# Optimization experiments

Hardware: AMD Instinct MI355X
Metric: run time of the kernel (lower is better)

## Reference

```python
import jax, jax.numpy as jnp
import numpy as np

N = 4096        # number of nodes
C = 512         # in_features
L_LAT = 64      # L_latent
EPS = 0.25      # epsilon


def setup_inputs() -> dict:
    key = jax.random.key(0)
    ks = jax.random.split(key, 8)
    def lin(k, fan_in, shape):
        return (jax.random.normal(k, shape, jnp.float32) / np.float32(np.sqrt(fan_in)))
    x = jax.random.normal(ks[0], (N, C), jnp.float32)
    adj = jax.random.uniform(ks[1], (N, N), jnp.float32)  # dense nonneg kernel
    W_proj = lin(ks[2], C, (C, L_LAT)); b_proj = jnp.zeros((L_LAT,), jnp.float32)
    W_pi1 = lin(ks[3], L_LAT, (L_LAT, C)); b_pi1 = jnp.zeros((C,), jnp.float32)
    W_pi2 = lin(ks[4], C, (C, 1)); b_pi2 = jnp.zeros((1,), jnp.float32)
    W_f = lin(ks[5], C, (C, C)); b_f = jnp.zeros((C,), jnp.float32)
    dt = jnp.array([0.1], jnp.float32)
    return {"x": x, "adj": adj, "W_proj": W_proj, "b_proj": b_proj,
            "W_pi1": W_pi1, "b_pi1": b_pi1, "W_pi2": W_pi2, "b_pi2": b_pi2,
            "W_f": W_f, "b_f": b_f, "dt": dt}


def reference(x, adj, W_proj, b_proj, W_pi1, b_pi1, W_pi2, b_pi2, W_f, b_f, dt):
    # proj_list: x -> latent [n, L]
    z = x @ W_proj + b_proj
    # pi_list: Linear -> ReLU -> Linear -> Sigmoid, squeeze to [n]
    pi = jax.nn.sigmoid(jax.nn.relu(z @ W_pi1 + b_pi1) @ W_pi2 + b_pi2)[:, 0]
    # q_epsilon_tilde: row sums of the kernel
    q = adj.sum(axis=1)                       # [n]
    # K_tilde = K_epsilon @ diag(pi/q)  == column scaling
    K_tilde = adj * (pi / q)[None, :]         # [n, n]
    # D_tilde diagonal; torch.inverse of a diagonal == elementwise reciprocal
    d = K_tilde.sum(axis=1) + 1e-5            # [n]
    # target = relu(f(x)) with f = Linear(C, C)
    target = jax.nn.relu(x @ W_f + b_f)       # [n, C]
    # L @ target = (1/eps) * diag(1/d) @ K_tilde @ target - target
    Lt = (K_tilde @ target) / (EPS * d)[:, None] - target
    return target + dt[0] * Lt
```

## Files before the change

kernel.cpp:

```cpp
#include <hip/hip_runtime.h>
#include <hip/hip_bf16.h>

#define N_NODES 4096
#define C_DIM   512
#define L_DIM   64
#define SPLITS  8
#define KCHUNK  (N_NODES / SPLITS)

typedef unsigned short u16;
typedef unsigned int   u32;
using bf16x8 = __attribute__((ext_vector_type(8))) __bf16;
using u16x8  = __attribute__((ext_vector_type(8))) unsigned short;
using f32x4  = __attribute__((ext_vector_type(4))) float;

__device__ __forceinline__ float b2f(u16 u) {
    union { unsigned int i; float f; } v; v.i = ((unsigned int)u) << 16; return v.f;
}
__device__ __forceinline__ u16 f2b(float f) {
    __bf16 h = (__bf16)f;
    union { __bf16 h; u16 u; } v; v.h = h; return v.u;
}
__device__ __forceinline__ void gload16(const void* g, void* l) {
    __builtin_amdgcn_global_load_lds((const __attribute__((address_space(1))) void*)g,
                                     (__attribute__((address_space(3))) void*)l,
                                     16, 0, 0);
}
__device__ __forceinline__ int detect_mode_inl(const u16* __restrict__ adj) {
    int m = 0;
#pragma unroll
    for (int i = 0; i < 64; ++i) m |= (adj[i] >= 0x8000) ? 1 : 0;
    return m;
}
__device__ __forceinline__ float ldin(const void* p, int i, int mode) {
    if (mode) return ((const float*)p)[i];
    return b2f(((const u16*)p)[i]);
}

#define OFF_MODE  0
#define OFF_DT    64
#define OFF_BIAS  1024
#define OFF_BP    4096
#define OFF_BP1   4608
#define OFF_WP2   8192
#define OFF_BP2   10240
#define OFF_Q     16384
#define OFF_S     32768
#define OFF_DV    49152
#define OFF_WPP   65536
#define OFF_WP1P  131072
#define OFF_WFT   196608
#define OFF_TST   9437184
#define OFF_XB    13631488
#define OFF_ADJB  17825792

__global__ __launch_bounds__(256) void k1_prep(const void* __restrict__ adj, const void* __restrict__ x,
        const void* Wp, const void* bp, const void* Wp1, const void* bp1,
        const void* Wp2, const void* bp2, const void* Wf, const void* bfc, const void* dt,
        int* __restrict__ modep,
        float* __restrict__ bp_f, float* __restrict__ bp1_f,
        float* __restrict__ Wp2_f, float* __restrict__ bp2_f,
        float* __restrict__ bias_f, float* __restrict__ dt_f,
        u32* __restrict__ WpP, u32* __restrict__ Wp1P,
        u16* __restrict__ adjb, float* __restrict__ q, u16* __restrict__ xb,
        u16* __restrict__ WfT) {
    __shared__ float tile[32][33];
    int bid = blockIdx.x, tid = threadIdx.x;
    int mode = detect_mode_inl((const u16*)adj);
    if (bid < 1024) {
        int wave = tid >> 6, lane = tid & 63;
        int row = bid * 4 + wave;
        float acc = 0.f;
        if (mode) {
            const float4* rp = (const float4*)((const float*)adj + (size_t)row * N_NODES);
            ushort4* wp = (ushort4*)(adjb + (size_t)row * N_NODES);
#pragma unroll 8
            for (int it = 0; it < 16; ++it) {
                float4 v = rp[it * 64 + lane];
                acc += (v.x + v.y) + (v.z + v.w);
                ushort4 o; o.x = f2b(v.x); o.y = f2b(v.y); o.z = f2b(v.z); o.w = f2b(v.w);
                wp[it * 64 + lane] = o;
            }
        } else {
            const u16x8* rp = (const u16x8*)((const u16*)adj + (size_t)row * N_NODES);
#pragma unroll
            for (int it = 0; it < 8; ++it) {
                u16x8 v = rp[it * 64 + lane];
#pragma unroll
                for (int e = 0; e < 8; ++e) acc += b2f(v[e]);
            }
        }
#pragma unroll
        for (int off = 32; off > 0; off >>= 1) acc += __shfl_down(acc, off);
        if (lane == 0) q[row] = acc;
    } else if (bid < 3072) {
        if (mode == 0) return;
        int idx = (bid - 1024) * 256 + tid;
        float4 v = ((const float4*)x)[idx];
        ushort4 o; o.x = f2b(v.x); o.y = f2b(v.y); o.z = f2b(v.z); o.w = f2b(v.w);
        ((ushort4*)xb)[idx] = o;
    } else if (bid < 3328) {
        int g = bid - 3072;
        int tx = tid & 31, ty = tid >> 5;
        int x0 = (g & 15) * 32, y0 = (g >> 4) * 32;
        if (mode) {
            const float* src = (const float*)Wf;
#pragma unroll
            for (int r = ty; r < 32; r += 8) tile[r][tx] = src[(size_t)(y0 + r) * C_DIM + x0 + tx];
        } else {
            const u16* src = (const u16*)Wf;
#pragma unroll
            for (int r = ty; r < 32; r += 8) tile[r][tx] = b2f(src[(size_t)(y0 + r) * C_DIM + x0 + tx]);
        }
        __syncthreads();
#pragma unroll
        for (int r = ty; r < 32; r += 8)
            WfT[(size_t)(x0 + r) * C_DIM + y0 + tx] = f2b(tile[tx][r]);
    } else if (bid < 3392) {
        int idx = (bid - 3328) * 256 + tid;
        int k2i = idx >> 6, j = idx & 63;
        float a = ldin(Wp, (2 * k2i) * L_DIM + j, mode);
        float b = ldin(Wp, (2 * k2i + 1) * L_DIM + j, mode);
        WpP[idx] = (u32)f2b(a) | ((u32)f2b(b) << 16);
    } else if (bid < 3456) {
        int idx = (bid - 3392) * 256 + tid;
        int jj2 = idx >> 9, m = idx & 511;
        float a = ldin(Wp1, (2 * jj2) * C_DIM + m, mode);
        float b = ldin(Wp1, (2 * jj2 + 1) * C_DIM + m, mode);
        Wp1P[idx] = (u32)f2b(a) | ((u32)f2b(b) << 16);
    } else {
        if (bid == 3456 && tid == 0) *modep = mode;
        int idx = (bid - 3456) * 256 + tid;
        if (idx < 64)           bp_f[idx]          = ldin(bp,  idx, mode);
        else if (idx < 576)     bp1_f[idx - 64]    = ldin(bp1, idx - 64, mode);
        else if (idx < 1088)    Wp2_f[idx - 576]   = ldin(Wp2, idx - 576, mode);
        else if (idx == 1088)   bp2_f[0]           = ldin(bp2, 0, mode);
        else if (idx < 1601)    bias_f[idx - 1089] = ldin(bfc, idx - 1089, mode);
        else if (idx == 1601)   dt_f[0]            = ldin(dt, 0, mode);
    }
}

__global__ __launch_bounds__(256) void k1p_pi(const void* __restrict__ xraw,
        const int* __restrict__ modep, const u16* __restrict__ xb,
        const u32* __restrict__ WpP, const u32* __restrict__ Wp1P,
        const float* __restrict__ bp_f,  const float* __restrict__ bp1_f,
        const float* __restrict__ Wp2_f, const float* __restrict__ bp2_f,
        const float* __restrict__ q, float* __restrict__ s) {
    __shared__ __align__(16) char smem[26880];
    int bid = blockIdx.x, tid = threadIdx.x;
    int mode = *modep;
    float (*sx)[C_DIM]      = (float(*)[C_DIM])smem;
    float (*red)[8][L_DIM]  = (float(*)[8][L_DIM])(smem + 16384);
    float (*sz)[L_DIM]      = (float(*)[L_DIM])(smem + 24576);
    float (*rw)[8]          = (float(*)[8])(smem + 26624);
    int i0 = bid * 8;
    const u16* xsrc = mode ? xb : (const u16*)xraw;
    const u16x8* xp = (const u16x8*)(xsrc + (size_t)i0 * C_DIM);
#pragma unroll
    for (int r = 0; r < 2; ++r) {
        u16x8 v = xp[tid + 256 * r];
        float* dstf = &sx[0][0] + (size_t)(tid + 256 * r) * 8;
#pragma unroll
        for (int e = 0; e < 8; ++e) dstf[e] = b2f(v[e]);
    }
    __syncthreads();
    int j = tid & 63, part = tid >> 6;
    float za[8];
#pragma unroll
    for (int n = 0; n < 8; ++n) za[n] = 0.f;
    const u32* wp = WpP + part * 4096 + j;
#pragma unroll 8
    for (int kk = 0; kk < 64; ++kk) {
        u32 w = wp[kk * 64];
        float wa = b2f((u16)(w & 0xFFFF)), wb = b2f((u16)(w >> 16));
        int k = part * 128 + kk * 2;
#pragma unroll
        for (int n = 0; n < 8; ++n) za[n] += sx[n][k] * wa + sx[n][k + 1] * wb;
    }
#pragma unroll
    for (int n = 0; n < 8; ++n) red[part][n][j] = za[n];
    __syncthreads();
#pragma unroll
    for (int r = 0; r < 2; ++r) {
        int idx = tid + r * 256; int n = idx >> 6, jj = idx & 63;
        sz[n][jj] = red[0][n][jj] + red[1][n][jj] + red[2][n][jj] + red[3][n][jj] + bp_f[jj];
    }
    __syncthreads();
    int m0 = tid, m1 = tid + 256;
    float h0[8], h1[8];
    float b0 = bp1_f[m0], b1 = bp1_f[m1];
#pragma unroll
    for (int n = 0; n < 8; ++n) { h0[n] = b0; h1[n] = b1; }
    const u32* w1p = Wp1P + m0;
#pragma unroll 4
    for (int jj2 = 0; jj2 < 32; ++jj2) {
        u32 w0 = w1p[jj2 * 512], w1 = w1p[jj2 * 512 + 256];
        float w0a = b2f((u16)(w0 & 0xFFFF)), w0b = b2f((u16)(w0 >> 16));
        float w1a = b2f((u16)(w1 & 0xFFFF)), w1b = b2f((u16)(w1 >> 16));
#pragma unroll
        for (int n = 0; n < 8; ++n) {
            float za_ = sz[n][2 * jj2], zb_ = sz[n][2 * jj2 + 1];
            h0[n] += za_ * w0a + zb_ * w0b;
            h1[n] += za_ * w1a + zb_ * w1b;
        }
    }
    float w2a = Wp2_f[m0], w2b = Wp2_f[m1];
    float p[8];
#pragma unroll
    for (int n = 0; n < 8; ++n)
        p[n] = fmaxf(h0[n], 0.f) * w2a + fmaxf(h1[n], 0.f) * w2b;
#pragma unroll
    for (int off = 32; off > 0; off >>= 1)
#pragma unroll
        for (int n = 0; n < 8; ++n) p[n] += __shfl_down(p[n], off);
    int lane = tid & 63, wave = tid >> 6;
    if (lane == 0) {
#pragma unroll
        for (int n = 0; n < 8; ++n) rw[wave][n] = p[n];
    }
    __syncthreads();
    if (tid < 8) {
        float tot = rw[0][tid] + rw[1][tid] + rw[2][tid] + rw[3][tid] + bp2_f[0];
        float pi = 1.f / (1.f + expf(-tot));
        s[i0 + tid] = pi / q[i0 + tid];
    }
}

__global__ __launch_bounds__(256) void k2_mid(const void* __restrict__ adjraw, const void* __restrict__ xraw,
        const int* __restrict__ modep,
        const float* __restrict__ s, const float* __restrict__ bias_f, const float* __restrict__ dt_f,
        const u16* __restrict__ adjb, const u16* __restrict__ xb, const u16* __restrict__ WfT,
        float* __restrict__ dv, u16* __restrict__ TsT,
        void* __restrict__ out, float* __restrict__ Pacc) {
    __shared__ __align__(16) char smem[16640];
    int bid = blockIdx.x, tid = threadIdx.x;
    int mode = *modep;
    if (bid < 1024) {
        float* s_lds = (float*)smem;
#pragma unroll
        for (int r = 0; r < 4; ++r) ((float4*)s_lds)[tid + 256 * r] = ((const float4*)s)[tid + 256 * r];
        __syncthreads();
        const u16* A = mode ? adjb : (const u16*)adjraw;
        int wave = tid >> 6, lane = tid & 63;
        int row = bid * 4 + wave;
        const u16x8* rp = (const u16x8*)(A + (size_t)row * N_NODES);
        float acc = 0.f;
#pragma unroll
        for (int it = 0; it < 8; ++it) {
            int chunk = it * 64 + lane;
            u16x8 v = rp[chunk];
            const float4* sp = (const float4*)(s_lds + chunk * 8);
            float4 s0 = sp[0], s1 = sp[1];
            acc += b2f(v[0]) * s0.x + b2f(v[1]) * s0.y + b2f(v[2]) * s0.z + b2f(v[3]) * s0.w;
            acc += b2f(v[4]) * s1.x + b2f(v[5]) * s1.y + b2f(v[6]) * s1.z + b2f(v[7]) * s1.w;
        }
#pragma unroll
        for (int off = 32; off > 0; off >>= 1) acc += __shfl_down(acc, off);
        if (lane == 0) dv[row] = 1.f / (acc + 1e-5f);
    } else {
        u16* lA = (u16*)smem;
        u16* lB = (u16*)(smem + 8192);
        u16* lT = (u16*)smem;
        float* s_row = (float*)(smem + 16384);
        int g = bid - 1024;
        int lane = tid & 63, wave = tid >> 6;
        int bm = (g & 63) * 64, bn = (g >> 6) * 64;
        if (tid < 64) s_row[tid] = s[bm + tid];
        const u16* Axb = mode ? xb : (const u16*)xraw;
        float* tgt = mode ? (float*)out : Pacc;
        int quad = lane >> 4, l15 = lane & 15;
        int wm = wave * 16;
        int trow = tid >> 3;
        int xslot = (tid & 7) ^ (trow & 7);
        const u16* Ap0 = Axb + (size_t)(bm + trow) * C_DIM + xslot * 8;
        const u16* Ap1 = Axb + (size_t)(bm + 32 + trow) * C_DIM + xslot * 8;
        const u16* Bp0 = WfT + (size_t)(bn + trow) * C_DIM + xslot * 8;
        const u16* Bp1 = WfT + (size_t)(bn + 32 + trow) * C_DIM + xslot * 8;
        f32x4 acc[4];
#pragma unroll
        for (int nt = 0; nt < 4; ++nt) acc[nt] = (f32x4){0.f, 0.f, 0.f, 0.f};
        for (int k0 = 0; k0 < C_DIM; k0 += 64) {
            gload16(Ap0 + k0, lA + tid * 8);
            gload16(Ap1 + k0, lA + 2048 + tid * 8);
            gload16(Bp0 + k0, lB + tid * 8);
            gload16(Bp1 + k0, lB + 2048 + tid * 8);
            asm volatile("s_waitcnt vmcnt(0)\n\ts_barrier" ::: "memory");
            __builtin_amdgcn_sched_barrier(0);
#pragma unroll
            for (int kk = 0; kk < 2; ++kk) {
                int xr = (((kk << 2) | quad) ^ (l15 & 7)) * 8;
                bf16x8 af = *(const bf16x8*)&lA[(wm + l15) * 64 + xr];
                bf16x8 bfv[4];
#pragma unroll
                for (int nt = 0; nt < 4; ++nt)
                    bfv[nt] = *(const bf16x8*)&lB[(nt * 16 + l15) * 64 + xr];
#pragma unroll
                for (int nt = 0; nt < 4; ++nt)
                    acc[nt] = __builtin_amdgcn_mfma_f32_16x16x32_bf16(af, bfv[nt], acc[nt], 0, 0, 0);
            }
            asm volatile("s_waitcnt lgkmcnt(0)\n\ts_barrier" ::: "memory");
        }
        float c0 = 1.f - dt_f[0];
#pragma unroll
        for (int nt = 0; nt < 4; ++nt) {
            int col_l = nt * 16 + l15;
            float bv = bias_f[bn + col_l];
#pragma unroll
            for (int r = 0; r < 4; ++r) {
                int row_l = wm + quad * 4 + r;
                float t = fmaxf(acc[nt][r] + bv, 0.f);
                tgt[(size_t)(bm + row_l) * C_DIM + bn + col_l] = c0 * t;
                lT[col_l * 64 + row_l] = f2b(t * s_row[row_l]);
            }
        }
        __syncthreads();
        int col_l = tid >> 2, seg = tid & 3;
        uint4 w0 = *(const uint4*)&lT[col_l * 64 + seg * 16];
        uint4 w1 = *(const uint4*)&lT[col_l * 64 + seg * 16 + 8];
        u16* dst = TsT + (size_t)(bn + col_l) * N_NODES + bm + seg * 16;
        *(uint4*)dst = w0;
        *(uint4*)(dst + 8) = w1;
    }
}

__global__ __launch_bounds__(256) void k3_gemm2(const void* __restrict__ adjraw,
        const int* __restrict__ modep,
        const u16* __restrict__ adjb, const u16* __restrict__ TsT,
        const float* __restrict__ dv, const float* __restrict__ dt_f,
        void* __restrict__ out, float* __restrict__ Pacc) {
    __shared__ __align__(16) u16 lA[8192];
    __shared__ __align__(16) u16 lB[8192];
    int mode = *modep;
    const u16* A = mode ? adjb : (const u16*)adjraw;
    float* tgt = mode ? (float*)out : Pacc;
    int tid = threadIdx.x;
    int lane = tid & 63, wave = tid >> 6;
    int id = blockIdx.x;
    int nid = (id & 7) * 128 + (id >> 3);
    int kbase = (nid & 7) * KCHUNK;
    int bn = ((nid >> 3) & 3) * 128;
    int bm = (nid >> 5) * 128;
    int wm = (wave & 1) * 64, wn = (wave >> 1) * 64;
    int quad = lane >> 4, l15 = lane & 15;
    int trow = tid >> 3;
    int xslot = (tid & 7) ^ (trow & 7);

    const u16* Ap[4]; const u16* Bp[4];
#pragma unroll
    for (int i = 0; i < 4; ++i) {
        Ap[i] = A   + (size_t)(bm + i * 32 + trow) * N_NODES + kbase + xslot * 8;
        Bp[i] = TsT + (size_t)(bn + i * 32 + trow) * N_NODES + kbase + xslot * 8;
    }

    f32x4 acc[4][4];
#pragma unroll
    for (int a = 0; a < 4; ++a)
#pragma unroll
        for (int b = 0; b < 4; ++b) acc[a][b] = (f32x4){0.f, 0.f, 0.f, 0.f};

    for (int k0 = 0; k0 < KCHUNK; k0 += 64) {
#pragma unroll
        for (int i = 0; i < 4; ++i) gload16(Ap[i] + k0, lA + i * 2048 + tid * 8);
#pragma unroll
        for (int i = 0; i < 4; ++i) gload16(Bp[i] + k0, lB + i * 2048 + tid * 8);
        asm volatile("s_waitcnt vmcnt(0)\n\ts_barrier" ::: "memory");
        __builtin_amdgcn_sched_barrier(0);
#pragma unroll
        for (int kk = 0; kk < 2; ++kk) {
            int xr = (((kk << 2) | quad) ^ (l15 & 7)) * 8;
            bf16x8 af[4], bfv[4];
#pragma unroll
            for (int mt = 0; mt < 4; ++mt) af[mt] = *(const bf16x8*)&lA[(wm + mt * 16 + l15) * 64 + xr];
#pragma unroll
            for (int nt = 0; nt < 4; ++nt) bfv[nt] = *(const bf16x8*)&lB[(wn + nt * 16 + l15) * 64 + xr];
#pragma unroll
            for (int mt = 0; mt < 4; ++mt)
#pragma unroll
                for (int nt = 0; nt < 4; ++nt)
                    acc[mt][nt] = __builtin_amdgcn_mfma_f32_16x16x32_bf16(af[mt], bfv[nt], acc[mt][nt], 0, 0, 0);
        }
        asm volatile("s_waitcnt lgkmcnt(0)\n\ts_barrier" ::: "memory");
    }

    float c1 = dt_f[0] * 4.f;
#pragma unroll
    for (int mt = 0; mt < 4; ++mt) {
        float inv[4];
#pragma unroll
        for (int r = 0; r < 4; ++r) inv[r] = c1 * dv[bm + wm + mt * 16 + quad * 4 + r];
#pragma unroll
        for (int nt = 0; nt < 4; ++nt) {
            int col = bn + wn + nt * 16 + l15;
#pragma unroll
            for (int r = 0; r < 4; ++r) {
                int row = bm + wm + mt * 16 + quad * 4 + r;
                atomicAdd(&tgt[(size_t)row * C_DIM + col], acc[mt][nt][r] * inv[r]);
            }
        }
    }
}

__global__ __launch_bounds__(256) void k5_fin(const int* __restrict__ modep,
                                              const float* __restrict__ Pacc,
                                              u16* __restrict__ out) {
    if (*modep) return;
    int idx = blockIdx.x * 256 + threadIdx.x;
    float4 v = ((const float4*)Pacc)[idx];
    ushort4 o; o.x = f2b(v.x); o.y = f2b(v.y); o.z = f2b(v.z); o.w = f2b(v.w);
    ((ushort4*)out)[idx] = o;
}

extern "C" void kernel_launch(void* const* d_in, const int* in_sizes, int n_in,
                              void* d_out, int out_size, void* d_ws, size_t ws_size,
                              hipStream_t stream) {
    const void* x   = d_in[0];
    const void* adj = d_in[1];
    const void* Wp  = d_in[2];
    const void* bp  = d_in[3];
    const void* Wp1 = d_in[4];
    const void* bp1 = d_in[5];
    const void* Wp2 = d_in[6];
    const void* bp2 = d_in[7];
    const void* Wf  = d_in[8];
    const void* bfc = d_in[9];
    const void* dtp = d_in[10];

    char* ws = (char*)d_ws;
    int*   modep  = (int*)(ws + OFF_MODE);
    float* dt_f   = (float*)(ws + OFF_DT);
    float* bias_f = (float*)(ws + OFF_BIAS);
    float* bp_f   = (float*)(ws + OFF_BP);
    float* bp1_f  = (float*)(ws + OFF_BP1);
    float* Wp2_f  = (float*)(ws + OFF_WP2);
    float* bp2_f  = (float*)(ws + OFF_BP2);
    float* q      = (float*)(ws + OFF_Q);
    float* s      = (float*)(ws + OFF_S);
    float* dv     = (float*)(ws + OFF_DV);
    u32*   WpP    = (u32*)(ws + OFF_WPP);
    u32*   Wp1P   = (u32*)(ws + OFF_WP1P);
    u16*   WfT    = (u16*)(ws + OFF_WFT);
    u16*   TsT    = (u16*)(ws + OFF_TST);
    u16*   xb     = (u16*)(ws + OFF_XB);
    u16*   adjb   = (u16*)(ws + OFF_ADJB);
    float* Pacc   = (float*)(ws + OFF_ADJB);

    k1_prep<<<3463, 256, 0, stream>>>(adj, x, Wp, bp, Wp1, bp1, Wp2, bp2, Wf, bfc, dtp,
                                      modep, bp_f, bp1_f, Wp2_f, bp2_f, bias_f, dt_f,
                                      WpP, Wp1P, adjb, q, xb, WfT);
    k1p_pi<<<512, 256, 0, stream>>>(x, modep, xb, WpP, Wp1P, bp_f, bp1_f, Wp2_f, bp2_f, q, s);
    k2_mid<<<1536, 256, 0, stream>>>(adj, x, modep, s, bias_f, dt_f, adjb, xb, WfT,
                                     dv, TsT, d_out, Pacc);
    k3_gemm2<<<1024, 256, 0, stream>>>(adj, modep, adjb, TsT, dv, dt_f, d_out, Pacc);
    k5_fin<<<2048, 256, 0, stream>>>(modep, Pacc, (u16*)d_out);
}
```

Baseline: 240.2 us.

## Fuse row-scaled reduction into GEMM2 pass and defer 1/d scaling to finalizer

Moves the K_tilde row-sum reduction (dv) from the mid kernel into extra blocks of the adjacency GEMM, accumulated with atomics, so the adj read for dv overlaps with the GEMM instead of running before it. GEMM2 now atomically accumulates unscaled partial products into a separate fp32 buffer, and the finalizer applies the per-row 1/d scale and adds the base term. Split-K is reduced from 8 to 4, giving 512 GEMM blocks plus 128 reduction blocks. The cost is zero-initialising the accumulator buffers in the prep kernel and always running a full finalizer pass, including in fp32 mode.

```diff
diff --git a/kernel.cpp b/kernel.cpp
--- a/kernel.cpp
+++ b/kernel.cpp
@@ -4,7 +4,7 @@
 #define N_NODES 4096
 #define C_DIM   512
 #define L_DIM   64
-#define SPLITS  8
+#define SPLITS  4
 #define KCHUNK  (N_NODES / SPLITS)
 
 typedef unsigned short u16;
@@ -49,6 +49,7 @@
 #define OFF_WPP   65536
 #define OFF_WP1P  131072
 #define OFF_WFT   196608
+#define OFF_PACC  720896
 #define OFF_TST   9437184
 #define OFF_XB    13631488
 #define OFF_ADJB  17825792
@@ -62,7 +63,7 @@
         float* __restrict__ bias_f, float* __restrict__ dt_f,
         u32* __restrict__ WpP, u32* __restrict__ Wp1P,
         u16* __restrict__ adjb, float* __restrict__ q, u16* __restrict__ xb,
-        u16* __restrict__ WfT) {
+        u16* __restrict__ WfT, float* __restrict__ Pacc2, float* __restrict__ dvraw) {
     __shared__ float tile[32][33];
     int bid = blockIdx.x, tid = threadIdx.x;
     int mode = detect_mode_inl((const u16*)adj);
@@ -127,7 +128,7 @@
         float a = ldin(Wp1, (2 * jj2) * C_DIM + m, mode);
         float b = ldin(Wp1, (2 * jj2 + 1) * C_DIM + m, mode);
         Wp1P[idx] = (u32)f2b(a) | ((u32)f2b(b) << 16);
-    } else {
+    } else if (bid < 3463) {
         if (bid == 3456 && tid == 0) *modep = mode;
         int idx = (bid - 3456) * 256 + tid;
         if (idx < 64)           bp_f[idx]          = ldin(bp,  idx, mode);
@@ -136,6 +137,12 @@
         else if (idx == 1088)   bp2_f[0]           = ldin(bp2, 0, mode);
         else if (idx < 1601)    bias_f[idx - 1089] = ldin(bfc, idx - 1089, mode);
         else if (idx == 1601)   dt_f[0]            = ldin(dt, 0, mode);
+    } else if (bid < 5511) {
+        int idx = (bid - 3463) * 256 + tid;
+        ((float4*)Pacc2)[idx] = make_float4(0.f, 0.f, 0.f, 0.f);
+    } else {
+        int idx = (bid - 5511) * 256 + tid;
+        dvraw[idx] = 0.f;
     }
 }
 
@@ -225,188 +232,199 @@
     }
 }
 
-__global__ __launch_bounds__(256) void k2_mid(const void* __restrict__ adjraw, const void* __restrict__ xraw,
+__global__ __launch_bounds__(256) void k2_gemm1(const void* __restrict__ xraw,
         const int* __restrict__ modep,
         const float* __restrict__ s, const float* __restrict__ bias_f, const float* __restrict__ dt_f,
-        const u16* __restrict__ adjb, const u16* __restrict__ xb, const u16* __restrict__ WfT,
-        float* __restrict__ dv, u16* __restrict__ TsT,
-        void* __restrict__ out, float* __restrict__ Pacc) {
+        const u16* __restrict__ xb, const u16* __restrict__ WfT,
+        u16* __restrict__ TsT, void* __restrict__ out, float* __restrict__ Pacc_base) {
     __shared__ __align__(16) char smem[16640];
     int bid = blockIdx.x, tid = threadIdx.x;
     int mode = *modep;
-    if (bid < 1024) {
-        float* s_lds = (float*)smem;
-#pragma unroll
-        for (int r = 0; r < 4; ++r) ((float4*)s_lds)[tid + 256 * r] = ((const float4*)s)[tid + 256 * r];
-        __syncthreads();
-        const u16* A = mode ? adjb : (const u16*)adjraw;
-        int wave = tid >> 6, lane = tid & 63;
-        int row = bid * 4 + wave;
-        const u16x8* rp = (const u16x8*)(A + (size_t)row * N_NODES);
-        float acc = 0.f;
-#pragma unroll
-        for (int it = 0; it < 8; ++it) {
-            int chunk = it * 64 + lane;
-            u16x8 v = rp[chunk];
-            const float4* sp = (const float4*)(s_lds + chunk * 8);
-            float4 s0 = sp[0], s1 = sp[1];
-            acc += b2f(v[0]) * s0.x + b2f(v[1]) * s0.y + b2f(v[2]) * s0.z + b2f(v[3]) * s0.w;
-            acc += b2f(v[4]) * s1.x + b2f(v[5]) * s1.y + b2f(v[6]) * s1.z + b2f(v[7]) * s1.w;
-        }
-#pragma unroll
-        for (int off = 32; off > 0; off >>= 1) acc += __shfl_down(acc, off);
-        if (lane == 0) dv[row] = 1.f / (acc + 1e-5f);
-    } else {
-        u16* lA = (u16*)smem;
-        u16* lB = (u16*)(smem + 8192);
-        u16* lT = (u16*)smem;
-        float* s_row = (float*)(smem + 16384);
-        int g = bid - 1024;
-        int lane = tid & 63, wave = tid >> 6;
-        int bm = (g & 63) * 64, bn = (g >> 6) * 64;
-        if (tid < 64) s_row[tid] = s[bm + tid];
-        const u16* Axb = mode ? xb : (const u16*)xraw;
-        float* tgt = mode ? (float*)out : Pacc;
-        int quad = lane >> 4, l15 = lane & 15;
-        int wm = wave * 16;
-        int trow = tid >> 3;
-        int xslot = (tid & 7) ^ (trow & 7);
-        const u16* Ap0 = Axb + (size_t)(bm + trow) * C_DIM + xslot * 8;
-        const u16* Ap1 = Axb + (size_t)(bm + 32 + trow) * C_DIM + xslot * 8;
-        const u16* Bp0 = WfT + (size_t)(bn + trow) * C_DIM + xslot * 8;
-        const u16* Bp1 = WfT + (size_t)(bn + 32 + trow) * C_DIM + xslot * 8;
-        f32x4 acc[4];
-#pragma unroll
-        for (int nt = 0; nt < 4; ++nt) acc[nt] = (f32x4){0.f, 0.f, 0.f, 0.f};
-        for (int k0 = 0; k0 < C_DIM; k0 += 64) {
-            gload16(Ap0 + k0, lA + tid * 8);
-            gload16(Ap1 + k0, lA + 2048 + tid * 8);
-            gload16(Bp0 + k0, lB + tid * 8);
-            gload16(Bp1 + k0, lB + 2048 + tid * 8);
-            asm volatile("s_waitcnt vmcnt(0)\n\ts_barrier" ::: "memory");
-            __builtin_amdgcn_sched_barrier(0);
-#pragma unroll
-            for (int kk = 0; kk < 2; ++kk) {
-                int xr = (((kk << 2) | quad) ^ (l15 & 7)) * 8;
-                bf16x8 af = *(const bf16x8*)&lA[(wm + l15) * 64 + xr];
-                bf16x8 bfv[4];
-#pragma unroll
-                for (int nt = 0; nt < 4; ++nt)
-                    bfv[nt] = *(const bf16x8*)&lB[(nt * 16 + l15) * 64 + xr];
-#pragma unroll
-                for (int nt = 0; nt < 4; ++nt)
-                    acc[nt] = __builtin_amdgcn_mfma_f32_16x16x32_bf16(af, bfv[nt], acc[nt], 0, 0, 0);
-            }
-            asm volatile("s_waitcnt lgkmcnt(0)\n\ts_barrier" ::: "memory");
-        }
-        float c0 = 1.f - dt_f[0];
-#pragma unroll
-        for (int nt = 0; nt < 4; ++nt) {
-            int col_l = nt * 16 + l15;
-            float bv = bias_f[bn + col_l];
-#pragma unroll
-            for (int r = 0; r < 4; ++r) {
-                int row_l = wm + quad * 4 + r;
-                float t = fmaxf(acc[nt][r] + bv, 0.f);
-                tgt[(size_t)(bm + row_l) * C_DIM + bn + col_l] = c0 * t;
-                lT[col_l * 64 + row_l] = f2b(t * s_row[row_l]);
-            }
-        }
-        __syncthreads();
-        int col_l = tid >> 2, seg = tid & 3;
-        uint4 w0 = *(const uint4*)&lT[col_l * 64 + seg * 16];
-        uint4 w1 = *(const uint4*)&lT[col_l * 64 + seg * 16 + 8];
-        u16* dst = TsT + (size_t)(bn + col_l) * N_NODES + bm + seg * 16;
-        *(uint4*)dst = w0;
-        *(uint4*)(dst + 8) = w1;
-    }
+    u16* lA = (u16*)smem;
+    u16* lB = (u16*)(smem + 8192);
+    u16* lT = (u16*)smem;
+    float* s_row = (float*)(smem + 16384);
+    int lane = tid & 63, wave = tid >> 6;
+    int bm = (bid & 63) * 64, bn = (bid >> 6) * 64;
+    if (tid < 64) s_row[tid] = s[bm + tid];
+    const u16* Axb = mode ? xb : (const u16*)xraw;
+    float* basep = mode ? (float*)out : Pacc_base;
+    int quad = lane >> 4, l15 = lane & 15;
+    int wm = wave * 16;
+    int trow = tid >> 3;
+    int xslot = (tid & 7) ^ (trow & 7);
+    const u16* Ap0 = Axb + (size_t)(bm + trow) * C_DIM + xslot * 8;
+    const u16* Ap1 = Axb + (size_t)(bm + 32 + trow) * C_DIM + xslot * 8;
+    const u16* Bp0 = WfT + (size_t)(bn + trow) * C_DIM + xslot * 8;
+    const u16* Bp1 = WfT + (size_t)(bn + 32 + trow) * C_DIM + xslot * 8;
+    f32x4 acc[4];
+#pragma unroll
+    for (int nt = 0; nt < 4; ++nt) acc[nt] = (f32x4){0.f, 0.f, 0.f, 0.f};
+    for (int k0 = 0; k0 < C_DIM; k0 += 64) {
+        gload16(Ap0 + k0, lA + tid * 8);
+        gload16(Ap1 + k0, lA + 2048 + tid * 8);
+        gload16(Bp0 + k0, lB + tid * 8);
+        gload16(Bp1 + k0, lB + 2048 + tid * 8);
+        asm volatile("s_waitcnt vmcnt(0)\n\ts_barrier" ::: "memory");
+        __builtin_amdgcn_sched_barrier(0);
+#pragma unroll
+        for (int kk = 0; kk < 2; ++kk) {
+            int xr = (((kk << 2) | quad) ^ (l15 & 7)) * 8;
+            bf16x8 af = *(const bf16x8*)&lA[(wm + l15) * 64 + xr];
+            bf16x8 bfv[4];
+#pragma unroll
+            for (int nt = 0; nt < 4; ++nt)
+                bfv[nt] = *(const bf16x8*)&lB[(nt * 16 + l15) * 64 + xr];
+#pragma unroll
+            for (int nt = 0; nt < 4; ++nt)
+                acc[nt] = __builtin_amdgcn_mfma_f32_16x16x32_bf16(af, bfv[nt], acc[nt], 0, 0, 0);
+        }
+        asm volatile("s_waitcnt lgkmcnt(0)\n\ts_barrier" ::: "memory");
+    }
+    float c0 = 1.f - dt_f[0];
+#pragma unroll
+    for (int nt = 0; nt < 4; ++nt) {
+        int col_l = nt * 16 + l15;
+        float bv = bias_f[bn + col_l];
+#pragma unroll
+        for (int r = 0; r < 4; ++r) {
+            int row_l = wm + quad * 4 + r;
+            float t = fmaxf(acc[nt][r] + bv, 0.f);
+            basep[(size_t)(bm + row_l) * C_DIM + bn + col_l] = c0 * t;
+            lT[col_l * 64 + row_l] = f2b(t * s_row[row_l]);
+        }
+    }
+    __syncthreads();
+    int col_l = tid >> 2, seg = tid & 3;
+    uint4 w0 = *(const uint4*)&lT[col_l * 64 + seg * 16];
+    uint4 w1 = *(const uint4*)&lT[col_l * 64 + seg * 16 + 8];
+    u16* dst = TsT + (size_t)(bn + col_l) * N_NODES + bm + seg * 16;
+    *(uint4*)dst = w0;
+    *(uint4*)(dst + 8) = w1;
 }
 
 __global__ __launch_bounds__(256) void k3_gemm2(const void* __restrict__ adjraw,
         const int* __restrict__ modep,
         const u16* __restrict__ adjb, const u16* __restrict__ TsT,
-        const float* __restrict__ dv, const float* __restrict__ dt_f,
-        void* __restrict__ out, float* __restrict__ Pacc) {
+        const float* __restrict__ s,
+        float* __restrict__ Pacc2, float* __restrict__ dvraw) {
     __shared__ __align__(16) u16 lA[8192];
     __shared__ __align__(16) u16 lB[8192];
     int mode = *modep;
     const u16* A = mode ? adjb : (const u16*)adjraw;
-    float* tgt = mode ? (float*)out : Pacc;
     int tid = threadIdx.x;
-    int lane = tid & 63, wave = tid >> 6;
     int id = blockIdx.x;
-    int nid = (id & 7) * 128 + (id >> 3);
-    int kbase = (nid & 7) * KCHUNK;
-    int bn = ((nid >> 3) & 3) * 128;
-    int bm = (nid >> 5) * 128;
-    int wm = (wave & 1) * 64, wn = (wave >> 1) * 64;
-    int quad = lane >> 4, l15 = lane & 15;
-    int trow = tid >> 3;
-    int xslot = (tid & 7) ^ (trow & 7);
-
-    const u16* Ap[4]; const u16* Bp[4];
-#pragma unroll
-    for (int i = 0; i < 4; ++i) {
-        Ap[i] = A   + (size_t)(bm + i * 32 + trow) * N_NODES + kbase + xslot * 8;
-        Bp[i] = TsT + (size_t)(bn + i * 32 + trow) * N_NODES + kbase + xslot * 8;
-    }
-
-    f32x4 acc[4][4];
-#pragma unroll
-    for (int a = 0; a < 4; ++a)
-#pragma unroll
-        for (int b = 0; b < 4; ++b) acc[a][b] = (f32x4){0.f, 0.f, 0.f, 0.f};
-
-    for (int k0 = 0; k0 < KCHUNK; k0 += 64) {
-#pragma unroll
-        for (int i = 0; i < 4; ++i) gload16(Ap[i] + k0, lA + i * 2048 + tid * 8);
-#pragma unroll
-        for (int i = 0; i < 4; ++i) gload16(Bp[i] + k0, lB + i * 2048 + tid * 8);
-        asm volatile("s_waitcnt vmcnt(0)\n\ts_barrier" ::: "memory");
-        __builtin_amdgcn_sched_barrier(0);
-#pragma unroll
-        for (int kk = 0; kk < 2; ++kk) {
-            int xr = (((kk << 2) | quad) ^ (l15 & 7)) * 8;
-            bf16x8 af[4], bfv[4];
-#pragma unroll
-            for (int mt = 0; mt < 4; ++mt) af[mt] = *(const bf16x8*)&lA[(wm + mt * 16 + l15) * 64 + xr];
-#pragma unroll
-            for (int nt = 0; nt < 4; ++nt) bfv[nt] = *(const bf16x8*)&lB[(wn + nt * 16 + l15) * 64 + xr];
-#pragma unroll
-            for (int mt = 0; mt < 4; ++mt)
-#pragma unroll
-                for (int nt = 0; nt < 4; ++nt)
-                    acc[mt][nt] = __builtin_amdgcn_mfma_f32_16x16x32_bf16(af[mt], bfv[nt], acc[mt][nt], 0, 0, 0);
-        }
-        asm volatile("s_waitcnt lgkmcnt(0)\n\ts_barrier" ::: "memory");
-    }
-
+    int xcd = id & 7, local = id >> 3;
+    if (local < 64) {
+        int lane = tid & 63, wave = tid >> 6;
+        int bm128 = (xcd * 4 + (local >> 4)) * 128;
+        int bn128 = ((local >> 2) & 3) * 128;
+        int kbase = (local & 3) * KCHUNK;
+        int wm = (wave & 1) * 64, wn = (wave >> 1) * 64;
+        int quad = lane >> 4, l15 = lane & 15;
+        int trow = tid >> 3;
+        int xslot = (tid & 7) ^ (trow & 7);
+
+        const u16* Ap[4]; const u16* Bp[4];
+#pragma unroll
+        for (int i = 0; i < 4; ++i) {
+            Ap[i] = A   + (size_t)(bm128 + i * 32 + trow) * N_NODES + kbase + xslot * 8;
+            Bp[i] = TsT + (size_t)(bn128 + i * 32 + trow) * N_NODES + kbase + xslot * 8;
+        }
+
+        f32x4 acc[4][4];
+#pragma unroll
+        for (int a = 0; a < 4; ++a)
+#pragma unroll
+            for (int b = 0; b < 4; ++b) acc[a][b] = (f32x4){0.f, 0.f, 0.f, 0.f};
+
+        for (int k0 = 0; k0 < KCHUNK; k0 += 64) {
+#pragma unroll
+            for (int i = 0; i < 4; ++i) gload16(Ap[i] + k0, lA + i * 2048 + tid * 8);
+#pragma unroll
+            for (int i = 0; i < 4; ++i) gload16(Bp[i] + k0, lB + i * 2048 + tid * 8);
+            asm volatile("s_waitcnt vmcnt(0)\n\ts_barrier" ::: "memory");
+            __builtin_amdgcn_sched_barrier(0);
+#pragma unroll
+            for (int kk = 0; kk < 2; ++kk) {
+                int xr = (((kk << 2) | quad) ^ (l15 & 7)) * 8;
+                bf16x8 af[4], bfv[4];
+#pragma unroll
+                for (int mt = 0; mt < 4; ++mt) af[mt] = *(const bf16x8*)&lA[(wm + mt * 16 + l15) * 64 + xr];
+#pragma unroll
+                for (int nt = 0; nt < 4; ++nt) bfv[nt] = *(const bf16x8*)&lB[(wn + nt * 16 + l15) * 64 + xr];
+#pragma unroll
+                for (int mt = 0; mt < 4; ++mt)
+#pragma unroll
+                    for (int nt = 0; nt < 4; ++nt)
+                        acc[mt][nt] = __builtin_amdgcn_mfma_f32_16x16x32_bf16(af[mt], bfv[nt], acc[mt][nt], 0, 0, 0);
+            }
+            asm volatile("s_waitcnt lgkmcnt(0)\n\ts_barrier" ::: "memory");
+        }
+
+#pragma unroll
+        for (int mt = 0; mt < 4; ++mt) {
+#pragma unroll
+            for (int nt = 0; nt < 4; ++nt) {
+                int col = bn128 + wn + nt * 16 + l15;
+#pragma unroll
+                for (int r = 0; r < 4; ++r) {
+                    int row = bm128 + wm + mt * 16 + quad * 4 + r;
+                    atomicAdd(&Pacc2[(size_t)row * C_DIM + col], acc[mt][nt][r]);
+                }
+            }
+        }
+    } else {
+        int l2 = local - 64;
+        int bm128 = (xcd * 4 + (l2 >> 2)) * 128;
+        int kbase = (l2 & 3) * KCHUNK;
+        float* s_lds = (float*)lA;
+        ((float4*)s_lds)[tid] = ((const float4*)(s + kbase))[tid];
+        __syncthreads();
+        int lane = tid & 63, wave = tid >> 6;
+        const u16* base_row = A + (size_t)(bm128 + wave * 32) * N_NODES + kbase;
+        for (int r = 0; r < 32; ++r) {
+            const u16x8* rp = (const u16x8*)(base_row + (size_t)r * N_NODES) + lane;
+            float acc = 0.f;
+#pragma unroll
+            for (int it = 0; it < 2; ++it) {
+                u16x8 v = rp[it * 64];
+                const float* sp = s_lds + it * 512 + lane * 8;
+#pragma unroll
+                for (int e = 0; e < 8; ++e) acc += b2f(v[e]) * sp[e];
+            }
+#pragma unroll
+            for (int off = 32; off > 0; off >>= 1) acc += __shfl_down(acc, off);
+            if (lane == 0) atomicAdd(&dvraw[bm128 + wave * 32 + r], acc);
+        }
+    }
+}
+
+__global__ __launch_bounds__(256) void k5_fin(const int* __restrict__ modep,
+                                              const float* __restrict__ dt_f,
+                                              const float* __restrict__ Pacc2,
+                                              const float* __restrict__ dvraw,
+                                              const float* __restrict__ Pacc_base,
+                                              void* __restrict__ out) {
+    int mode = *modep;
+    int idx = blockIdx.x * 256 + threadIdx.x;
     float c1 = dt_f[0] * 4.f;
-#pragma unroll
-    for (int mt = 0; mt < 4; ++mt) {
-        float inv[4];
-#pragma unroll
-        for (int r = 0; r < 4; ++r) inv[r] = c1 * dv[bm + wm + mt * 16 + quad * 4 + r];
-#pragma unroll
-        for (int nt = 0; nt < 4; ++nt) {
-            int col = bn + wn + nt * 16 + l15;
-#pragma unroll
-            for (int r = 0; r < 4; ++r) {
-                int row = bm + wm + mt * 16 + quad * 4 + r;
-                atomicAdd(&tgt[(size_t)row * C_DIM + col], acc[mt][nt][r] * inv[r]);
-            }
-        }
-    }
-}
-
-__global__ __launch_bounds__(256) void k5_fin(const int* __restrict__ modep,
-                                              const float* __restrict__ Pacc,
-                                              u16* __restrict__ out) {
-    if (*modep) return;
-    int idx = blockIdx.x * 256 + threadIdx.x;
-    float4 v = ((const float4*)Pacc)[idx];
-    ushort4 o; o.x = f2b(v.x); o.y = f2b(v.y); o.z = f2b(v.z); o.w = f2b(v.w);
-    ((ushort4*)out)[idx] = o;
+    const float4* basep = mode ? (const float4*)out : (const float4*)Pacc_base;
+    float4 b = basep[idx];
+    float4 p = ((const float4*)Pacc2)[idx];
+    int row = idx >> 7;
+    float rscale = c1 / (dvraw[row] + 1e-5f);
+    float4 v;
+    v.x = b.x + p.x * rscale;
+    v.y = b.y + p.y * rscale;
+    v.z = b.z + p.z * rscale;
+    v.w = b.w + p.w * rscale;
+    if (mode) {
+        ((float4*)out)[idx] = v;
+    } else {
+        ushort4 o; o.x = f2b(v.x); o.y = f2b(v.y); o.z = f2b(v.z); o.w = f2b(v.w);
+        ((ushort4*)out)[idx] = o;
+    }
 }
 
 extern "C" void kernel_launch(void* const* d_in, const int* in_sizes, int n_in,
@@ -434,21 +452,21 @@
     float* bp2_f  = (float*)(ws + OFF_BP2);
     float* q      = (float*)(ws + OFF_Q);
     float* s      = (float*)(ws + OFF_S);
-    float* dv     = (float*)(ws + OFF_DV);
+    float* dvraw  = (float*)(ws + OFF_DV);
     u32*   WpP    = (u32*)(ws + OFF_WPP);
     u32*   Wp1P   = (u32*)(ws + OFF_WP1P);
     u16*   WfT    = (u16*)(ws + OFF_WFT);
+    float* Pacc2  = (float*)(ws + OFF_PACC);
     u16*   TsT    = (u16*)(ws + OFF_TST);
     u16*   xb     = (u16*)(ws + OFF_XB);
     u16*   adjb   = (u16*)(ws + OFF_ADJB);
-    float* Pacc   = (float*)(ws + OFF_ADJB);
-
-    k1_prep<<<3463, 256, 0, stream>>>(adj, x, Wp, bp, Wp1, bp1, Wp2, bp2, Wf, bfc, dtp,
+    float* Pacc_base = (float*)(ws + OFF_ADJB);
+
+    k1_prep<<<5527, 256, 0, stream>>>(adj, x, Wp, bp, Wp1, bp1, Wp2, bp2, Wf, bfc, dtp,
                                       modep, bp_f, bp1_f, Wp2_f, bp2_f, bias_f, dt_f,
-                                      WpP, Wp1P, adjb, q, xb, WfT);
+                                      WpP, Wp1P, adjb, q, xb, WfT, Pacc2, dvraw);
     k1p_pi<<<512, 256, 0, stream>>>(x, modep, xb, WpP, Wp1P, bp_f, bp1_f, Wp2_f, bp2_f, q, s);
-    k2_mid<<<1536, 256, 0, stream>>>(adj, x, modep, s, bias_f, dt_f, adjb, xb, WfT,
-                                     dv, TsT, d_out, Pacc);
-    k3_gemm2<<<1024, 256, 0, stream>>>(adj, modep, adjb, TsT, dv, dt_f, d_out, Pacc);
-    k5_fin<<<2048, 256, 0, stream>>>(modep, Pacc, (u16*)d_out);
-}
+    k2_gemm1<<<512, 256, 0, stream>>>(x, modep, s, bias_f, dt_f, xb, WfT, TsT, d_out, Pacc_base);
+    k3_gemm2<<<640, 256, 0, stream>>>(adj, modep, adjb, TsT, s, Pacc2, dvraw);
+    k5_fin<<<2048, 256, 0, stream>>>(modep, dt_f, Pacc2, dvraw, Pacc_base, d_out);
+}
```

Result: faster. 234.5 us (-2.3%).
